# Optimization experiments

Measured on AMD Instinct MI355X. Metric: run time of the kernel, lower is better.

The kernel has to match this reference:

```python
import jax, jax.numpy as jnp
import numpy as np

TOP_K = 13
NUM_CLASSES = 80
ALPHA = 1.0
BETA = 6.0
EPS = 1e-9
IOU_EPS = 1e-7


def _ciou(box1, box2, eps=IOU_EPS):
    # box1: gt [B,M,1,4], box2: pred [B,1,A,4], corner format x1y1x2y2
    b1x1, b1y1, b1x2, b1y2 = jnp.split(box1, 4, axis=-1)
    b2x1, b2y1, b2x2, b2y2 = jnp.split(box2, 4, axis=-1)
    w1, h1 = b1x2 - b1x1, b1y2 - b1y1 + eps
    w2, h2 = b2x2 - b2x1, b2y2 - b2y1 + eps
    inter = (jnp.clip(jnp.minimum(b1x2, b2x2) - jnp.maximum(b1x1, b2x1), 0, None)
             * jnp.clip(jnp.minimum(b1y2, b2y2) - jnp.maximum(b1y1, b2y1), 0, None))
    union = w1 * h1 + w2 * h2 - inter + eps
    iou = inter / union
    cw = jnp.maximum(b1x2, b2x2) - jnp.minimum(b1x1, b2x1)  # enclosing box
    ch = jnp.maximum(b1y2, b2y2) - jnp.minimum(b1y1, b2y1)
    c2 = cw ** 2 + ch ** 2 + eps
    rho2 = ((b2x1 + b2x2 - b1x1 - b1x2) ** 2 + (b2y1 + b2y2 - b1y1 - b1y2) ** 2) / 4.0
    v = (4.0 / np.pi ** 2) * (jnp.arctan(w2 / h2) - jnp.arctan(w1 / h1)) ** 2
    alpha = v / (v - iou + (1.0 + eps))
    return (iou - (rho2 / c2 + v * alpha))[..., 0]  # [B,M,A]


def _assign(pred_cls, pred_bbox, anchor_points, gt_cls, gt_bbox, mask_gt):
    B, A, C = pred_cls.shape
    M = gt_bbox.shape[1]
    # --- anchors inside gt boxes: [B,M,A] ---
    lt, rb = gt_bbox[:, :, None, :2], gt_bbox[:, :, None, 2:]   # [B,M,1,2]
    xy = anchor_points[None, None]                               # [1,1,A,2]
    deltas = jnp.concatenate([xy - lt, rb - xy], axis=-1)        # [B,M,A,4]
    mask_in_gts = (deltas.min(-1) > EPS).astype(pred_bbox.dtype)
    mask = mask_in_gts * mask_gt                                 # mask_gt [B,M,1] broadcasts
    # --- box metrics: gather class scores at gt labels, full CIoU grid masked ---
    labels = gt_cls[..., 0].astype(jnp.int32)                    # [B,M]
    idx = jnp.broadcast_to(labels[:, None, :], (B, A, M))
    bbox_scores = jnp.take_along_axis(pred_cls, idx, axis=2).transpose(0, 2, 1) * mask
    overlaps = jnp.clip(_ciou(gt_bbox[:, :, None], pred_bbox[:, None]), 0, None) * mask
    align_metric = bbox_scores ** ALPHA * overlaps ** BETA       # [B,M,A]
    # --- top-k candidate selection (indices of masked-out gts forced to 0, dup counts zeroed) ---
    _, topk_idx = jax.lax.top_k(align_metric, TOP_K)             # [B,M,K]
    topk_mask = jnp.broadcast_to(mask_gt > 0, (B, M, TOP_K))
    topk_idx = jnp.where(topk_mask, topk_idx, 0)
    bi = jnp.arange(B)[:, None, None]
    mi = jnp.arange(M)[None, :, None]
    count = jnp.zeros((B, M, A), jnp.int32).at[bi, mi, topk_idx].add(1)
    mask_topk = jnp.where(count > 1, 0, count).astype(align_metric.dtype)
    mask_pos = mask_topk * mask_in_gts * mask_gt                 # [B,M,A]
    # --- resolve anchors claimed by multiple gts via max overlap ---
    fg = mask_pos.sum(-2)                                        # [B,A]
    is_max = jax.nn.one_hot(overlaps.argmax(1), M, dtype=mask_pos.dtype).transpose(0, 2, 1)
    mask_pos = jnp.where(fg[:, None, :] > 1, is_max, mask_pos)
    fg_mask = mask_pos.sum(-2)                                   # [B,A]
    target_gt_idx = mask_pos.argmax(-2)                          # [B,A]
    # --- gather targets ---
    flat = target_gt_idx + jnp.arange(B)[:, None] * M
    target_labels = labels.reshape(-1)[flat]                     # [B,A]
    target_bbox = gt_bbox.reshape(-1, 4)[flat]                   # [B,A,4]
    target_cls = jnp.where(fg_mask[..., None] > 0,
                           jax.nn.one_hot(target_labels, C, dtype=pred_cls.dtype), 0.0)
    # --- normalize scores by aligned metric ---
    align_metric = align_metric * mask_pos
    pos_align = align_metric.max(-1, keepdims=True)              # [B,M,1]
    pos_overlap = (overlaps * mask_pos).max(-1, keepdims=True)   # [B,M,1]
    norm = (align_metric * pos_overlap / (pos_align + EPS)).max(-2)[..., None]  # [B,A,1]
    target_cls = target_cls * norm
    return target_cls, target_bbox, fg_mask


def setup_inputs() -> dict:
    key = jax.random.key(0)
    ks = jax.random.split(key, 8)
    B, A, C, M = 16, 8400, 80, 32
    anchor_points = jax.random.uniform(ks[0], (A, 2)) * 80.0
    pred_cls = jax.random.uniform(ks[1], (B, A, C))  # sigmoid-like scores in [0,1)
    ctr = anchor_points[None] + jax.random.normal(ks[2], (B, A, 2)) * 2.0
    sz = jax.random.uniform(ks[3], (B, A, 2)) * 15.0 + 2.0
    pred_bbox = jnp.concatenate([ctr - sz / 2, ctr + sz / 2], axis=-1)
    gctr = jax.random.uniform(ks[4], (B, M, 2)) * 80.0
    gsz = jax.random.uniform(ks[5], (B, M, 2)) * 25.0 + 3.0
    gt_bbox = jnp.concatenate([gctr - gsz / 2, gctr + gsz / 2], axis=-1)
    gt_cls = jax.random.randint(ks[6], (B, M, 1), 0, C).astype(jnp.int64)
    mask_gt = (jax.random.uniform(ks[7], (B, M, 1)) < 0.8).astype(jnp.float32)
    return {"pred_cls": pred_cls, "pred_bbox": pred_bbox, "anchor_points": anchor_points,
            "gt_cls": gt_cls, "gt_bbox": gt_bbox, "mask_gt": mask_gt}


def reference(pred_cls, pred_bbox, anchor_points, gt_cls, gt_bbox, mask_gt):
    target_cls, target_bbox, fg_mask = _assign(pred_cls, pred_bbox, anchor_points,
                                               gt_cls, gt_bbox, mask_gt)
    return target_cls, target_bbox, fg_mask.astype(bool)
```

## Files before the change

kernel.cpp:

```cpp
#include <hip/hip_runtime.h>
#include <cstdint>
#include <cstddef>

#define BB 16
#define AA 8400
#define CC 80
#define MM 32
#define TOPK 13
#define NW 8
#define WORDS 264
#define CWORDS 33
#define CANCH (CWORDS * 32)

__device__ __forceinline__ float ciou_clip(
    float gx1, float gy1, float gx2, float gy2, float at1,
    float4 pb, float w2, float h2, float at2)
{
  const float w1 = gx2 - gx1, h1 = gy2 - gy1 + 1e-7f;
  const float iw = fmaxf(fminf(gx2, pb.z) - fmaxf(gx1, pb.x), 0.f);
  const float ih = fmaxf(fminf(gy2, pb.w) - fmaxf(gy1, pb.y), 0.f);
  const float inter = iw * ih;
  const float uni = w1*h1 + w2*h2 - inter + 1e-7f;
  const float iou = inter / uni;
  const float cw = fmaxf(gx2, pb.z) - fminf(gx1, pb.x);
  const float ch = fmaxf(gy2, pb.w) - fminf(gy1, pb.y);
  const float c2 = cw*cw + ch*ch + 1e-7f;
  const float rx = pb.x + pb.z - gx1 - gx2;
  const float ry = pb.y + pb.w - gy1 - gy2;
  const float rho2 = (rx*rx + ry*ry) * 0.25f;
  const float dv = at2 - at1;
  const float v = 0.4052847345693511f * dv * dv;
  const float alpha = v / (v - iou + (1.f + 1e-7f));
  return fmaxf(iou - (rho2 / c2 + v * alpha), 0.f);
}

__device__ __forceinline__ unsigned long long pack_key(float val, int a) {
  return ((unsigned long long)__float_as_uint(val) << 32)
       | (unsigned long long)(0xFFFFFFFFu - (unsigned)a);
}
__device__ __forceinline__ int key_anchor(unsigned long long k) {
  return (int)(0xFFFFFFFFu - (unsigned)(k & 0xFFFFFFFFull));
}

__global__ __launch_bounds__(256) void k_mask(
    const float* __restrict__ anchors, const float* __restrict__ gt_bbox,
    const float* __restrict__ mask_gt, unsigned int* __restrict__ inmaskT,
    unsigned int* __restrict__ claim,
    unsigned int* __restrict__ pos_align, unsigned int* __restrict__ pos_ovl)
{
  const int b = blockIdx.y;
  __shared__ float4 s_mb[MM];
  if (threadIdx.x < MM) {
    const int m = threadIdx.x;
    const float4 g = reinterpret_cast<const float4*>(gt_bbox)[b*MM + m];
    s_mb[m] = (mask_gt[b*MM + m] > 0.f) ? g
              : make_float4(1e30f, 1e30f, -1e30f, -1e30f);
    if (blockIdx.x == 0) { pos_align[b*MM + m] = 0u; pos_ovl[b*MM + m] = 0u; }
  }
  __syncthreads();
  const int a = blockIdx.x*256 + threadIdx.x;
  const int wave = threadIdx.x >> 6, lane = threadIdx.x & 63;
  float2 xy = make_float2(-1e30f, -1e30f);
  if (a < AA) {
    xy = reinterpret_cast<const float2*>(anchors)[a];
    claim[b*AA + a] = 0u;
  }
  const int wslot = blockIdx.x*8 + wave*2;
  #pragma unroll
  for (int m = 0; m < MM; ++m) {
    const float4 g = s_mb[m];
    const float mind = fminf(fminf(xy.x - g.x, xy.y - g.y),
                             fminf(g.z - xy.x, g.w - xy.y));
    const unsigned long long bal = __ballot(mind > 1e-9f);
    unsigned int* wp = inmaskT + (size_t)(b*MM + m)*WORDS + wslot;
    if (lane == 0) wp[0] = (unsigned int)(bal & 0xffffffffull);
    if (lane == 1) wp[1] = (unsigned int)(bal >> 32);
  }
}

__global__ __launch_bounds__(512) void k_topk(
    const float* __restrict__ pred_cls, const float* __restrict__ pred_bbox,
    const float* __restrict__ anchors, const int* __restrict__ gt_cls,
    const float* __restrict__ gt_bbox, const float* __restrict__ mask_gt,
    const unsigned int* __restrict__ inmaskT, unsigned int* __restrict__ claim)
{
  const int m = blockIdx.x, b = blockIdx.y;
  if (mask_gt[b*MM + m] <= 0.f) return;
  const int wave = threadIdx.x >> 6, lane = threadIdx.x & 63;
  __shared__ unsigned short q[NW][CANCH];
  __shared__ unsigned long long s_top[NW][TOPK];

  const float4 gb = reinterpret_cast<const float4*>(gt_bbox)[b*MM + m];
  const float at1 = atanf((gb.z - gb.x) / (gb.w - gb.y + 1e-7f));
  const int lbl = gt_cls[b*MM + m];
  const float*  clsbase = pred_cls + (size_t)b*AA*CC;
  const float4* pbase   = reinterpret_cast<const float4*>(pred_bbox) + (size_t)b*AA;
  const float2* axy     = reinterpret_cast<const float2*>(anchors);

  unsigned long long k13[TOPK];
  #pragma unroll
  for (int i = 0; i < TOPK; ++i) k13[i] = 0ull;

  if (wave == 0) {
    const int a = lane;
    const float2 xy = axy[a];
    const float mind = fminf(fminf(xy.x - gb.x, xy.y - gb.y),
                             fminf(gb.z - xy.x, gb.w - xy.y));
    float val = 0.f;
    if (mind > 1e-9f) {
      const float4 pb = pbase[a];
      const float w2 = pb.z - pb.x, h2 = pb.w - pb.y + 1e-7f;
      const float at2 = atanf(w2 / h2);
      const float ov = ciou_clip(gb.x, gb.y, gb.z, gb.w, at1, pb, w2, h2, at2);
      const float o2 = ov * ov;
      val = clsbase[(size_t)a*CC + lbl] * (o2 * o2 * o2);
    }
    k13[0] = pack_key(val, a);
  }

  const unsigned int* wrow = inmaskT + (size_t)(b*MM + m)*WORDS + wave*CWORDS;
  unsigned int w = 0u;
  if (lane < CWORDS) w = wrow[lane];
  if (wave == 0 && lane < 2) w = 0u;
  const int cnt = __popc(w);
  int incl = cnt;
  #pragma unroll
  for (int off = 1; off < 64; off <<= 1) {
    const int t = __shfl_up(incl, off);
    if (lane >= off) incl += t;
  }
  int pos = incl - cnt;
  {
    const int lbase = lane*32;
    unsigned int t = w;
    while (t) {
      const int bit = __ffs((int)t) - 1; t &= t - 1u;
      q[wave][pos++] = (unsigned short)(lbase + bit);
    }
  }
  const int qc = __shfl(incl, 63);

  const int abase = wave * CANCH;
  for (int k = lane; k < qc; k += 64) {
    const int a = abase + (int)q[wave][k];
    const float4 pb = pbase[a];
    const float w2 = pb.z - pb.x, h2 = pb.w - pb.y + 1e-7f;
    const float at2 = atanf(w2 / h2);
    const float ov = ciou_clip(gb.x, gb.y, gb.z, gb.w, at1, pb, w2, h2, at2);
    const float o2 = ov * ov;
    const float val = clsbase[(size_t)a*CC + lbl] * (o2 * o2 * o2);
    const unsigned long long key = pack_key(val, a);
    if (key > k13[TOPK-1]) {
      #pragma unroll
      for (int i = TOPK-1; i >= 1; --i)
        if (key > k13[i]) k13[i] = (key > k13[i-1]) ? k13[i-1] : key;
      if (key > k13[0]) k13[0] = key;
    }
  }

  for (int r = 0; r < TOPK; ++r) {
    unsigned long long bk = k13[0];
    #pragma unroll
    for (int off = 32; off; off >>= 1) {
      const unsigned long long o = __shfl_xor(bk, off);
      if (o > bk) bk = o;
    }
    if (k13[0] == bk) {
      #pragma unroll
      for (int i = 0; i < TOPK-1; ++i) k13[i] = k13[i+1];
      k13[TOPK-1] = 0ull;
    }
    if (lane == 0) s_top[wave][r] = bk;
  }
  __syncthreads();
  if (wave != 0) return;

  unsigned long long v0 = 0ull, v1 = 0ull;
  bool g0 = false, g1 = false;
  {
    const int e0 = lane, e1 = lane + 64;
    v0 = s_top[e0/TOPK][e0%TOPK];
    if (e1 < NW*TOPK) v1 = s_top[e1/TOPK][e1%TOPK];
    const int a0 = key_anchor(v0), a1 = key_anchor(v1);
    if ((unsigned)a0 < (unsigned)AA) {
      const float2 xy = axy[a0];
      g0 = fminf(fminf(xy.x - gb.x, xy.y - gb.y),
                 fminf(gb.z - xy.x, gb.w - xy.y)) > 1e-9f;
    }
    if ((unsigned)a1 < (unsigned)AA) {
      const float2 xy = axy[a1];
      g1 = fminf(fminf(xy.x - gb.x, xy.y - gb.y),
                 fminf(gb.z - xy.x, gb.w - xy.y)) > 1e-9f;
    }
  }
  const unsigned int bit = 1u << m;
  for (int r = 0; r < TOPK; ++r) {
    const bool s1 = v1 > v0;
    unsigned long long bk = s1 ? v1 : v0;
    const unsigned long long my = bk;
    #pragma unroll
    for (int off = 32; off; off >>= 1) {
      const unsigned long long o = __shfl_xor(bk, off);
      if (o > bk) bk = o;
    }
    if (my == bk && bk != 0ull) {
      const bool ing = s1 ? g1 : g0;
      if (ing) atomicOr(&claim[b*AA + key_anchor(bk)], bit);
      if (s1) { v1 = 0ull; g1 = false; } else { v0 = 0ull; g0 = false; }
    }
  }
}

__global__ __launch_bounds__(256) void k_resolve(
    const float* __restrict__ pred_cls, const float* __restrict__ pred_bbox,
    const float* __restrict__ anchors, const int* __restrict__ gt_cls,
    const float* __restrict__ gt_bbox, const float* __restrict__ mask_gt,
    const unsigned int* __restrict__ claim,
    float* __restrict__ out_bbox, float* __restrict__ out_fg,
    int* __restrict__ anchor_m, float* __restrict__ anchor_al,
    unsigned int* __restrict__ pos_align, unsigned int* __restrict__ pos_ovl)
{
  const int b = blockIdx.y;
  __shared__ float s_x1[MM], s_y1[MM], s_x2[MM], s_y2[MM], s_at[MM], s_mgt[MM];
  __shared__ int s_lbl[MM];
  if (threadIdx.x < MM) {
    int m = threadIdx.x;
    float4 g = reinterpret_cast<const float4*>(gt_bbox)[b*MM + m];
    s_x1[m] = g.x; s_y1[m] = g.y; s_x2[m] = g.z; s_y2[m] = g.w;
    s_at[m] = atanf((g.z - g.x) / (g.w - g.y + 1e-7f));
    s_lbl[m] = gt_cls[b*MM + m];
    s_mgt[m] = mask_gt[b*MM + m];
  }
  __syncthreads();
  const int a = blockIdx.x*256 + threadIdx.x;
  if (a >= AA) return;
  const unsigned int cb = claim[b*AA + a];
  const int fg = __popc(cb);
  int asg = -1; float bestov = 0.f;
  if (fg > 0) {
    const float4 pb = reinterpret_cast<const float4*>(pred_bbox)[b*AA + a];
    const float2 xy = reinterpret_cast<const float2*>(anchors)[a];
    const float w2 = pb.z - pb.x, h2 = pb.w - pb.y + 1e-7f;
    const float at2 = atanf(w2 / h2);
    if (fg == 1) {
      asg = __ffs(cb) - 1;
      bestov = ciou_clip(s_x1[asg], s_y1[asg], s_x2[asg], s_y2[asg], s_at[asg],
                         pb, w2, h2, at2);
    } else {
      float best = -1.f; int bm = 0;
      for (int m = 0; m < MM; ++m) {
        float ov = 0.f;
        const float mind = fminf(fminf(xy.x - s_x1[m], xy.y - s_y1[m]),
                                 fminf(s_x2[m] - xy.x, s_y2[m] - xy.y));
        if (mind > 1e-9f && s_mgt[m] > 0.f)
          ov = ciou_clip(s_x1[m], s_y1[m], s_x2[m], s_y2[m], s_at[m],
                         pb, w2, h2, at2);
        if (ov > best) { best = ov; bm = m; }
      }
      asg = bm; bestov = best;
    }
  }
  const int tgt = (asg >= 0) ? asg : 0;
  float4 tb; tb.x = s_x1[tgt]; tb.y = s_y1[tgt]; tb.z = s_x2[tgt]; tb.w = s_y2[tgt];
  reinterpret_cast<float4*>(out_bbox)[b*AA + a] = tb;
  out_fg[b*AA + a] = (asg >= 0) ? 1.f : 0.f;
  anchor_m[b*AA + a] = asg;
  float av = 0.f;
  if (asg >= 0) {
    const float o2 = bestov * bestov;
    av = pred_cls[(size_t)(b*AA + a)*CC + s_lbl[asg]] * (o2 * o2 * o2);
    atomicMax(&pos_align[b*MM + asg], __float_as_uint(av));
    atomicMax(&pos_ovl[b*MM + asg], __float_as_uint(bestov));
  }
  anchor_al[b*AA + a] = av;
}

__global__ __launch_bounds__(256) void k_cls(
    const int* __restrict__ anchor_m, const float* __restrict__ anchor_al,
    const unsigned int* __restrict__ pos_align, const unsigned int* __restrict__ pos_ovl,
    const int* __restrict__ gt_cls, float* __restrict__ out_cls)
{
  const int tid = blockIdx.x*256 + threadIdx.x;
  if (tid >= BB*AA*(CC/4)) return;
  const int q  = tid % (CC/4);
  const int ba = tid / (CC/4);
  const int b  = ba / AA;
  const int m  = anchor_m[ba];
  float4 o = make_float4(0.f, 0.f, 0.f, 0.f);
  if (m >= 0) {
    const float pa = __uint_as_float(pos_align[b*MM + m]);
    const float po = __uint_as_float(pos_ovl[b*MM + m]);
    const float norm = anchor_al[ba] * po / (pa + 1e-9f);
    const int lbl = gt_cls[b*MM + m];
    const int c0 = q * 4;
    if (lbl == c0    ) o.x = norm;
    if (lbl == c0 + 1) o.y = norm;
    if (lbl == c0 + 2) o.z = norm;
    if (lbl == c0 + 3) o.w = norm;
  }
  reinterpret_cast<float4*>(out_cls)[tid] = o;
}

extern "C" void kernel_launch(void* const* d_in, const int* in_sizes, int n_in,
                              void* d_out, int out_size, void* d_ws, size_t ws_size,
                              hipStream_t stream)
{
  const float* pred_cls  = (const float*)d_in[0];
  const float* pred_bbox = (const float*)d_in[1];
  const float* anchors   = (const float*)d_in[2];
  const int*   gt_cls    = (const int*)  d_in[3];
  const float* gt_bbox   = (const float*)d_in[4];
  const float* mask_gt   = (const float*)d_in[5];

  char* ws = (char*)d_ws;
  unsigned int* claim     = (unsigned int*)(ws);
  unsigned int* pos_align = (unsigned int*)(ws + 537600);
  unsigned int* pos_ovl   = (unsigned int*)(ws + 539648);
  int*   anchor_m  = (int*)  (ws + 541696);
  float* anchor_al = (float*)(ws + 1079296);
  unsigned int* inmaskT = (unsigned int*)(ws + 1616896);

  float* out_cls  = (float*)d_out;
  float* out_bbox = out_cls + (size_t)BB*AA*CC;
  float* out_fg   = out_bbox + (size_t)BB*AA*4;

  k_mask<<<dim3(33, BB), 256, 0, stream>>>(
      anchors, gt_bbox, mask_gt, inmaskT, claim, pos_align, pos_ovl);
  k_topk<<<dim3(MM, BB), 512, 0, stream>>>(
      pred_cls, pred_bbox, anchors, gt_cls, gt_bbox, mask_gt, inmaskT, claim);
  k_resolve<<<dim3((AA + 255)/256, BB), 256, 0, stream>>>(
      pred_cls, pred_bbox, anchors, gt_cls, gt_bbox, mask_gt, claim,
      out_bbox, out_fg, anchor_m, anchor_al, pos_align, pos_ovl);
  k_cls<<<(BB*AA*(CC/4) + 255)/256, 256, 0, stream>>>(
      anchor_m, anchor_al, pos_align, pos_ovl, gt_cls, out_cls);
}
```

Baseline: 50.01 us.

## Fuse four kernels into two: inline mask ballot, per-batch shared-memory assignment

Drops the separate mask-bitmap kernel. The top-k kernel now builds its candidate queue by computing the in-box test directly with ballots, and it also zero-fills the outputs (class scores, default bbox, fg). The resolve and class-scatter kernels are replaced by a single per-batch 1024-thread kernel. That kernel keeps claims, per-GT maxima and assignments in shared memory and scatters only the positive anchors into the pre-zeroed outputs. This removes launches, global atomics and intermediate buffers, but the assign kernel runs only 16 blocks, which limits parallelism.

Result: slower. 63.26 us (+26.5%).

```diff
diff --git a/kernel.cpp b/kernel.cpp
--- a/kernel.cpp
+++ b/kernel.cpp
@@ -8,9 +8,7 @@
 #define MM 32
 #define TOPK 13
 #define NW 8
-#define WORDS 264
-#define CWORDS 33
-#define CANCH (CWORDS * 32)
+#define CANCH 1056
 
 __device__ __forceinline__ float ciou_clip(
     float gx1, float gy1, float gx2, float gy2, float at1,
@@ -42,51 +40,40 @@
   return (int)(0xFFFFFFFFu - (unsigned)(k & 0xFFFFFFFFull));
 }
 
-__global__ __launch_bounds__(256) void k_mask(
-    const float* __restrict__ anchors, const float* __restrict__ gt_bbox,
-    const float* __restrict__ mask_gt, unsigned int* __restrict__ inmaskT,
-    unsigned int* __restrict__ claim,
-    unsigned int* __restrict__ pos_align, unsigned int* __restrict__ pos_ovl)
-{
-  const int b = blockIdx.y;
-  __shared__ float4 s_mb[MM];
-  if (threadIdx.x < MM) {
-    const int m = threadIdx.x;
-    const float4 g = reinterpret_cast<const float4*>(gt_bbox)[b*MM + m];
-    s_mb[m] = (mask_gt[b*MM + m] > 0.f) ? g
-              : make_float4(1e30f, 1e30f, -1e30f, -1e30f);
-    if (blockIdx.x == 0) { pos_align[b*MM + m] = 0u; pos_ovl[b*MM + m] = 0u; }
-  }
-  __syncthreads();
-  const int a = blockIdx.x*256 + threadIdx.x;
-  const int wave = threadIdx.x >> 6, lane = threadIdx.x & 63;
-  float2 xy = make_float2(-1e30f, -1e30f);
-  if (a < AA) {
-    xy = reinterpret_cast<const float2*>(anchors)[a];
-    claim[b*AA + a] = 0u;
-  }
-  const int wslot = blockIdx.x*8 + wave*2;
-  #pragma unroll
-  for (int m = 0; m < MM; ++m) {
-    const float4 g = s_mb[m];
-    const float mind = fminf(fminf(xy.x - g.x, xy.y - g.y),
-                             fminf(g.z - xy.x, g.w - xy.y));
-    const unsigned long long bal = __ballot(mind > 1e-9f);
-    unsigned int* wp = inmaskT + (size_t)(b*MM + m)*WORDS + wslot;
-    if (lane == 0) wp[0] = (unsigned int)(bal & 0xffffffffull);
-    if (lane == 1) wp[1] = (unsigned int)(bal >> 32);
-  }
-}
-
 __global__ __launch_bounds__(512) void k_topk(
     const float* __restrict__ pred_cls, const float* __restrict__ pred_bbox,
     const float* __restrict__ anchors, const int* __restrict__ gt_cls,
     const float* __restrict__ gt_bbox, const float* __restrict__ mask_gt,
-    const unsigned int* __restrict__ inmaskT, unsigned int* __restrict__ claim)
+    unsigned long long* __restrict__ topkeys,
+    float* __restrict__ out_cls, float* __restrict__ out_bbox,
+    float* __restrict__ out_fg)
 {
   const int m = blockIdx.x, b = blockIdx.y;
-  if (mask_gt[b*MM + m] <= 0.f) return;
-  const int wave = threadIdx.x >> 6, lane = threadIdx.x & 63;
+  const int tid = threadIdx.x;
+  const int wave = tid >> 6, lane = tid & 63;
+
+  {
+    const int span = AA*CC/4/MM;
+    float4* oc = reinterpret_cast<float4*>(out_cls)
+               + (size_t)b*(AA*CC/4) + (size_t)m*span;
+    const float4 z4 = make_float4(0.f, 0.f, 0.f, 0.f);
+    for (int k = tid; k < span; k += 512) oc[k] = z4;
+    if (m == 0) {
+      const float4 g0 = reinterpret_cast<const float4*>(gt_bbox)[b*MM];
+      float4* ob = reinterpret_cast<float4*>(out_bbox) + (size_t)b*AA;
+      for (int k = tid; k < AA; k += 512) ob[k] = g0;
+    } else if (m == 1) {
+      float* of = out_fg + (size_t)b*AA;
+      for (int k = tid; k < AA; k += 512) of[k] = 0.f;
+    }
+  }
+
+  unsigned long long* tk = topkeys + (size_t)(b*MM + m)*TOPK;
+  if (mask_gt[b*MM + m] <= 0.f) {
+    if (tid < TOPK) tk[tid] = 0ull;
+    return;
+  }
+
   __shared__ unsigned short q[NW][CANCH];
   __shared__ unsigned long long s_top[NW][TOPK];
 
@@ -118,29 +105,26 @@
     k13[0] = pack_key(val, a);
   }
 
-  const unsigned int* wrow = inmaskT + (size_t)(b*MM + m)*WORDS + wave*CWORDS;
-  unsigned int w = 0u;
-  if (lane < CWORDS) w = wrow[lane];
-  if (wave == 0 && lane < 2) w = 0u;
-  const int cnt = __popc(w);
-  int incl = cnt;
-  #pragma unroll
-  for (int off = 1; off < 64; off <<= 1) {
-    const int t = __shfl_up(incl, off);
-    if (lane >= off) incl += t;
-  }
-  int pos = incl - cnt;
-  {
-    const int lbase = lane*32;
-    unsigned int t = w;
-    while (t) {
-      const int bit = __ffs((int)t) - 1; t &= t - 1u;
-      q[wave][pos++] = (unsigned short)(lbase + bit);
-    }
-  }
-  const int qc = __shfl(incl, 63);
-
   const int abase = wave * CANCH;
+  int qc = 0;
+  for (int s = 0; s < 17; ++s) {
+    const int la = s*64 + lane;
+    const int a  = abase + la;
+    bool pass = false;
+    if (la < CANCH && a < AA && !(wave == 0 && a < 64)) {
+      const float2 xy = axy[a];
+      const float mind = fminf(fminf(xy.x - gb.x, xy.y - gb.y),
+                               fminf(gb.z - xy.x, gb.w - xy.y));
+      pass = mind > 1e-9f;
+    }
+    const unsigned long long bal = __ballot(pass);
+    if (pass) {
+      const int pos = qc + (int)__popcll(bal & ((1ull << lane) - 1ull));
+      q[wave][pos] = (unsigned short)la;
+    }
+    qc += (int)__popcll(bal);
+  }
+
   for (int k = lane; k < qc; k += 64) {
     const int a = abase + (int)q[wave][k];
     const float4 pb = pbase[a];
@@ -176,24 +160,11 @@
   if (wave != 0) return;
 
   unsigned long long v0 = 0ull, v1 = 0ull;
-  bool g0 = false, g1 = false;
   {
     const int e0 = lane, e1 = lane + 64;
     v0 = s_top[e0/TOPK][e0%TOPK];
     if (e1 < NW*TOPK) v1 = s_top[e1/TOPK][e1%TOPK];
-    const int a0 = key_anchor(v0), a1 = key_anchor(v1);
-    if ((unsigned)a0 < (unsigned)AA) {
-      const float2 xy = axy[a0];
-      g0 = fminf(fminf(xy.x - gb.x, xy.y - gb.y),
-                 fminf(gb.z - xy.x, gb.w - xy.y)) > 1e-9f;
-    }
-    if ((unsigned)a1 < (unsigned)AA) {
-      const float2 xy = axy[a1];
-      g1 = fminf(fminf(xy.x - gb.x, xy.y - gb.y),
-                 fminf(gb.z - xy.x, gb.w - xy.y)) > 1e-9f;
-    }
-  }
-  const unsigned int bit = 1u << m;
+  }
   for (int r = 0; r < TOPK; ++r) {
     const bool s1 = v1 > v0;
     unsigned long long bk = s1 ? v1 : v0;
@@ -203,102 +174,102 @@
       const unsigned long long o = __shfl_xor(bk, off);
       if (o > bk) bk = o;
     }
+    if (lane == 0) tk[r] = bk;
     if (my == bk && bk != 0ull) {
-      const bool ing = s1 ? g1 : g0;
-      if (ing) atomicOr(&claim[b*AA + key_anchor(bk)], bit);
-      if (s1) { v1 = 0ull; g1 = false; } else { v0 = 0ull; g0 = false; }
-    }
-  }
-}
-
-__global__ __launch_bounds__(256) void k_resolve(
+      if (s1) v1 = 0ull; else v0 = 0ull;
+    }
+  }
+}
+
+__global__ __launch_bounds__(1024) void k_assign(
     const float* __restrict__ pred_cls, const float* __restrict__ pred_bbox,
     const float* __restrict__ anchors, const int* __restrict__ gt_cls,
     const float* __restrict__ gt_bbox, const float* __restrict__ mask_gt,
-    const unsigned int* __restrict__ claim,
-    float* __restrict__ out_bbox, float* __restrict__ out_fg,
-    int* __restrict__ anchor_m, float* __restrict__ anchor_al,
-    unsigned int* __restrict__ pos_align, unsigned int* __restrict__ pos_ovl)
-{
-  const int b = blockIdx.y;
-  __shared__ float s_x1[MM], s_y1[MM], s_x2[MM], s_y2[MM], s_at[MM], s_mgt[MM];
+    const unsigned long long* __restrict__ topkeys,
+    float* __restrict__ out_cls, float* __restrict__ out_bbox,
+    float* __restrict__ out_fg)
+{
+  const int b = blockIdx.x;
+  const int tid = threadIdx.x;
+  __shared__ unsigned int s_claim[AA];
+  __shared__ float s_av[AA];
+  __shared__ unsigned char s_asg[AA];
+  __shared__ unsigned int s_pal[MM], s_pov[MM];
+  __shared__ float4 s_gb[MM];
+  __shared__ float s_at[MM], s_mgt[MM];
   __shared__ int s_lbl[MM];
-  if (threadIdx.x < MM) {
-    int m = threadIdx.x;
-    float4 g = reinterpret_cast<const float4*>(gt_bbox)[b*MM + m];
-    s_x1[m] = g.x; s_y1[m] = g.y; s_x2[m] = g.z; s_y2[m] = g.w;
-    s_at[m] = atanf((g.z - g.x) / (g.w - g.y + 1e-7f));
-    s_lbl[m] = gt_cls[b*MM + m];
-    s_mgt[m] = mask_gt[b*MM + m];
-  }
-  __syncthreads();
-  const int a = blockIdx.x*256 + threadIdx.x;
-  if (a >= AA) return;
-  const unsigned int cb = claim[b*AA + a];
-  const int fg = __popc(cb);
-  int asg = -1; float bestov = 0.f;
-  if (fg > 0) {
-    const float4 pb = reinterpret_cast<const float4*>(pred_bbox)[b*AA + a];
-    const float2 xy = reinterpret_cast<const float2*>(anchors)[a];
+
+  const float2* axy   = reinterpret_cast<const float2*>(anchors);
+  const float4* pbase = reinterpret_cast<const float4*>(pred_bbox) + (size_t)b*AA;
+
+  if (tid < MM) {
+    const float4 g = reinterpret_cast<const float4*>(gt_bbox)[b*MM + tid];
+    s_gb[tid] = g;
+    s_at[tid] = atanf((g.z - g.x) / (g.w - g.y + 1e-7f));
+    s_lbl[tid] = gt_cls[b*MM + tid];
+    s_mgt[tid] = mask_gt[b*MM + tid];
+    s_pal[tid] = 0u; s_pov[tid] = 0u;
+  }
+  for (int k = tid; k < AA; k += 1024) s_claim[k] = 0u;
+  __syncthreads();
+
+  if (tid < MM*TOPK) {
+    const int m = tid / TOPK;
+    const unsigned long long key = topkeys[(size_t)(b*MM + m)*TOPK + tid%TOPK];
+    const int a = key_anchor(key);
+    if ((unsigned)a < (unsigned)AA) {
+      const float2 xy = axy[a];
+      const float4 g = s_gb[m];
+      const float mind = fminf(fminf(xy.x - g.x, xy.y - g.y),
+                               fminf(g.z - xy.x, g.w - xy.y));
+      if (mind > 1e-9f) atomicOr(&s_claim[a], 1u << m);
+    }
+  }
+  __syncthreads();
+
+  for (int a = tid; a < AA; a += 1024) {
+    const unsigned cb = s_claim[a];
+    if (cb == 0u) continue;
+    const float4 pb = pbase[a];
+    const float2 xy = axy[a];
     const float w2 = pb.z - pb.x, h2 = pb.w - pb.y + 1e-7f;
     const float at2 = atanf(w2 / h2);
-    if (fg == 1) {
+    int asg; float bestov;
+    if (__popc(cb) == 1) {
       asg = __ffs(cb) - 1;
-      bestov = ciou_clip(s_x1[asg], s_y1[asg], s_x2[asg], s_y2[asg], s_at[asg],
-                         pb, w2, h2, at2);
+      const float4 g = s_gb[asg];
+      bestov = ciou_clip(g.x, g.y, g.z, g.w, s_at[asg], pb, w2, h2, at2);
     } else {
       float best = -1.f; int bm = 0;
       for (int m = 0; m < MM; ++m) {
         float ov = 0.f;
-        const float mind = fminf(fminf(xy.x - s_x1[m], xy.y - s_y1[m]),
-                                 fminf(s_x2[m] - xy.x, s_y2[m] - xy.y));
+        const float4 g = s_gb[m];
+        const float mind = fminf(fminf(xy.x - g.x, xy.y - g.y),
+                                 fminf(g.z - xy.x, g.w - xy.y));
         if (mind > 1e-9f && s_mgt[m] > 0.f)
-          ov = ciou_clip(s_x1[m], s_y1[m], s_x2[m], s_y2[m], s_at[m],
-                         pb, w2, h2, at2);
+          ov = ciou_clip(g.x, g.y, g.z, g.w, s_at[m], pb, w2, h2, at2);
         if (ov > best) { best = ov; bm = m; }
       }
       asg = bm; bestov = best;
     }
-  }
-  const int tgt = (asg >= 0) ? asg : 0;
-  float4 tb; tb.x = s_x1[tgt]; tb.y = s_y1[tgt]; tb.z = s_x2[tgt]; tb.w = s_y2[tgt];
-  reinterpret_cast<float4*>(out_bbox)[b*AA + a] = tb;
-  out_fg[b*AA + a] = (asg >= 0) ? 1.f : 0.f;
-  anchor_m[b*AA + a] = asg;
-  float av = 0.f;
-  if (asg >= 0) {
     const float o2 = bestov * bestov;
-    av = pred_cls[(size_t)(b*AA + a)*CC + s_lbl[asg]] * (o2 * o2 * o2);
-    atomicMax(&pos_align[b*MM + asg], __float_as_uint(av));
-    atomicMax(&pos_ovl[b*MM + asg], __float_as_uint(bestov));
-  }
-  anchor_al[b*AA + a] = av;
-}
-
-__global__ __launch_bounds__(256) void k_cls(
-    const int* __restrict__ anchor_m, const float* __restrict__ anchor_al,
-    const unsigned int* __restrict__ pos_align, const unsigned int* __restrict__ pos_ovl,
-    const int* __restrict__ gt_cls, float* __restrict__ out_cls)
-{
-  const int tid = blockIdx.x*256 + threadIdx.x;
-  if (tid >= BB*AA*(CC/4)) return;
-  const int q  = tid % (CC/4);
-  const int ba = tid / (CC/4);
-  const int b  = ba / AA;
-  const int m  = anchor_m[ba];
-  float4 o = make_float4(0.f, 0.f, 0.f, 0.f);
-  if (m >= 0) {
-    const float pa = __uint_as_float(pos_align[b*MM + m]);
-    const float po = __uint_as_float(pos_ovl[b*MM + m]);
-    const float norm = anchor_al[ba] * po / (pa + 1e-9f);
-    const int lbl = gt_cls[b*MM + m];
-    const int c0 = q * 4;
-    if (lbl == c0    ) o.x = norm;
-    if (lbl == c0 + 1) o.y = norm;
-    if (lbl == c0 + 2) o.z = norm;
-    if (lbl == c0 + 3) o.w = norm;
-  }
-  reinterpret_cast<float4*>(out_cls)[tid] = o;
+    const float av = pred_cls[(size_t)(b*AA + a)*CC + s_lbl[asg]] * (o2*o2*o2);
+    atomicMax(&s_pal[asg], __float_as_uint(av));
+    atomicMax(&s_pov[asg], __float_as_uint(bestov));
+    s_asg[a] = (unsigned char)asg;
+    s_av[a]  = av;
+  }
+  __syncthreads();
+
+  for (int a = tid; a < AA; a += 1024) {
+    if (s_claim[a] == 0u) continue;
+    const int asg = s_asg[a];
+    const float norm = s_av[a] * __uint_as_float(s_pov[asg])
+                     / (__uint_as_float(s_pal[asg]) + 1e-9f);
+    out_fg[b*AA + a] = 1.f;
+    reinterpret_cast<float4*>(out_bbox)[b*AA + a] = s_gb[asg];
+    out_cls[(size_t)(b*AA + a)*CC + s_lbl[asg]] = norm;
+  }
 }
 
 extern "C" void kernel_launch(void* const* d_in, const int* in_sizes, int n_in,
@@ -312,25 +283,16 @@
   const float* gt_bbox   = (const float*)d_in[4];
   const float* mask_gt   = (const float*)d_in[5];
 
-  char* ws = (char*)d_ws;
-  unsigned int* claim     = (unsigned int*)(ws);
-  unsigned int* pos_align = (unsigned int*)(ws + 537600);
-  unsigned int* pos_ovl   = (unsigned int*)(ws + 539648);
-  int*   anchor_m  = (int*)  (ws + 541696);
-  float* anchor_al = (float*)(ws + 1079296);
-  unsigned int* inmaskT = (unsigned int*)(ws + 1616896);
+  unsigned long long* topkeys = (unsigned long long*)d_ws;
 
   float* out_cls  = (float*)d_out;
   float* out_bbox = out_cls + (size_t)BB*AA*CC;
   float* out_fg   = out_bbox + (size_t)BB*AA*4;
 
-  k_mask<<<dim3(33, BB), 256, 0, stream>>>(
-      anchors, gt_bbox, mask_gt, inmaskT, claim, pos_align, pos_ovl);
   k_topk<<<dim3(MM, BB), 512, 0, stream>>>(
-      pred_cls, pred_bbox, anchors, gt_cls, gt_bbox, mask_gt, inmaskT, claim);
-  k_resolve<<<dim3((AA + 255)/256, BB), 256, 0, stream>>>(
-      pred_cls, pred_bbox, anchors, gt_cls, gt_bbox, mask_gt, claim,
-      out_bbox, out_fg, anchor_m, anchor_al, pos_align, pos_ovl);
-  k_cls<<<(BB*AA*(CC/4) + 255)/256, 256, 0, stream>>>(
-      anchor_m, anchor_al, pos_align, pos_ovl, gt_cls, out_cls);
-}
+      pred_cls, pred_bbox, anchors, gt_cls, gt_bbox, mask_gt,
+      topkeys, out_cls, out_bbox, out_fg);
+  k_assign<<<dim3(BB), 1024, 0, stream>>>(
+      pred_cls, pred_bbox, anchors, gt_cls, gt_bbox, mask_gt,
+      topkeys, out_cls, out_bbox, out_fg);
+}
```
